# Optimization experiments

Hardware: AMD Instinct MI355X
Metric: run time of the kernel (lower is better)

Reference implementation:

```python
import jax, jax.numpy as jnp
import numpy as np

C1, C2, RATIO = 512, 256, 16

def setup_inputs() -> dict:
    key = jax.random.key(0)
    k1, k2, k3 = jax.random.split(key, 3)
    x = jax.random.normal(k1, (32, C1, 64, 64), dtype=jnp.float32)
    # torch Linear(c1, c1//ratio, bias=False): weight [c1//ratio, c1]
    w1 = jax.random.normal(k2, (C1 // RATIO, C1), dtype=jnp.float32) * (1.0 / np.sqrt(C1))
    w2 = jax.random.normal(k3, (C1, C1 // RATIO), dtype=jnp.float32) * (1.0 / np.sqrt(C1 // RATIO))
    return {"x": x, "w1": w1, "w2": w2}

def reference(x, w1, w2):
    b, c, h, w = x.shape
    # global average pool -> [b, c]
    y = jnp.mean(x, axis=(2, 3))
    # SE MLP: relu(y @ w1.T) @ w2.T, then sigmoid
    y = jax.nn.sigmoid(jnp.einsum('br,cr->bc', jax.nn.relu(jnp.einsum('bc,rc->br', y, w1)), w2))
    # descending sort indices over channels, keep top c2
    idx = jnp.argsort(-y, axis=1)[:, :C2]            # [b, c2] int
    # per-batch channel gather: out[b] = x[b, idx[b]]
    out = jnp.take_along_axis(x, idx[:, :, None, None], axis=1)  # [b, c2, h, w]
    return out
```

## Files before the change

kernel.cpp:

```cpp
#include <hip/hip_runtime.h>
#include <hip/hip_bf16.h>
#include <math.h>


#define C1 512
#define C2 256
#define CMID 32
#define HW 4096
#define B 32
#define W1PAD 516

typedef float f32x4 __attribute__((ext_vector_type(4)));

__device__ float g_y[B * C1];
__device__ int   g_idx[B * C2];

__global__ __launch_bounds__(256) void pool_np_kernel(const float* __restrict__ x) {
    int bc = blockIdx.x * 4 + (threadIdx.x >> 6);
    int L = threadIdx.x & 63;
    const float* a = x + (size_t)bc * HW;
    const float* base = a + (L >> 1) * 128 + (L & 1) * 4;
    f32x4 r = *(const f32x4*)base;
#pragma unroll
    for (int i = 1; i < 16; ++i) {
        f32x4 v = *(const f32x4*)(base + 8 * i);
        r.x = __fadd_rn(r.x, v.x);
        r.y = __fadd_rn(r.y, v.y);
        r.z = __fadd_rn(r.z, v.z);
        r.w = __fadd_rn(r.w, v.w);
    }
    float s = __fadd_rn(__fadd_rn(r.x, r.y), __fadd_rn(r.z, r.w));
    s = __fadd_rn(s, __shfl_xor(s, 1));
    s = __fadd_rn(s, __shfl_xor(s, 2));
    s = __fadd_rn(s, __shfl_xor(s, 4));
    s = __fadd_rn(s, __shfl_xor(s, 8));
    s = __fadd_rn(s, __shfl_xor(s, 16));
    s = __fadd_rn(s, __shfl_xor(s, 32));
    if (L == 0) g_y[bc] = __fdiv_rn(s, 4096.0f);
}

__global__ __launch_bounds__(512) void se_np_kernel(const float* __restrict__ w1,
                                                    const float* __restrict__ w2) {
    int b = blockIdx.x;
    int t = threadIdx.x;
    __shared__ float ys[C1];
    __shared__ float hs[CMID];
    __shared__ float ss[C1];
    __shared__ float w1s[CMID * W1PAD];

    f32x4 w2r[8];
#pragma unroll
    for (int i = 0; i < 8; ++i)
        w2r[i] = ((const f32x4*)(w2 + t * CMID))[i];

#pragma unroll
    for (int i = 0; i < 8; ++i) {
        int u = i * 512 + t;
        int row  = u >> 7;
        int col4 = u & 127;
        f32x4 v = ((const f32x4*)w1)[u];
        *(f32x4*)&w1s[row * W1PAD + col4 * 4] = v;
    }
    ys[t] = g_y[b * C1 + t];
    __syncthreads();

    if (t < CMID * 4) {
        int row = t >> 2, k = t & 3;
        const float* wr = &w1s[row * W1PAD];
        float Lk = 0.f;
#pragma unroll
        for (int c = 0; c < C1; c += 8) {
            Lk = __fadd_rn(Lk, __fmul_rn(ys[c + k],     wr[c + k]));
            Lk = __fadd_rn(Lk, __fmul_rn(ys[c + 4 + k], wr[c + 4 + k]));
        }
        Lk = __fadd_rn(Lk, __shfl_xor(Lk, 1));
        Lk = __fadd_rn(Lk, __shfl_xor(Lk, 2));
        if (k == 0) hs[row] = Lk > 0.0f ? Lk : 0.0f;
    }
    __syncthreads();

    {
        float L0 = 0.f, L1 = 0.f, L2 = 0.f, L3 = 0.f;
#pragma unroll
        for (int i = 0; i < 8; i += 2) {
            L0 = __fadd_rn(L0, __fmul_rn(hs[i * 4 + 0], w2r[i].x));
            L1 = __fadd_rn(L1, __fmul_rn(hs[i * 4 + 1], w2r[i].y));
            L2 = __fadd_rn(L2, __fmul_rn(hs[i * 4 + 2], w2r[i].z));
            L3 = __fadd_rn(L3, __fmul_rn(hs[i * 4 + 3], w2r[i].w));
            L0 = __fadd_rn(L0, __fmul_rn(hs[i * 4 + 4], w2r[i + 1].x));
            L1 = __fadd_rn(L1, __fmul_rn(hs[i * 4 + 5], w2r[i + 1].y));
            L2 = __fadd_rn(L2, __fmul_rn(hs[i * 4 + 6], w2r[i + 1].z));
            L3 = __fadd_rn(L3, __fmul_rn(hs[i * 4 + 7], w2r[i + 1].w));
        }
        float z = __fadd_rn(__fadd_rn(L0, L1), __fadd_rn(L2, L3));
        float e = (float)exp((double)(-z));
        ss[t] = __fdiv_rn(1.0f, __fadd_rn(1.0f, e));
    }
    __syncthreads();

    float sc = ss[t];
    int rank = 0;
#pragma unroll 8
    for (int c = 0; c < C1; ++c) {
        float v = ss[c];
        rank += (int)((v > sc) || (v == sc && c < t));
    }
    if (rank < C2) g_idx[b * C2 + rank] = t;
}

__global__ __launch_bounds__(256) void gather_kernel(const float* __restrict__ x,
                                                     float* __restrict__ out) {
    int bid  = blockIdx.x >> 1;
    int half = blockIdx.x & 1;
    int b = bid >> 8;
    int c = g_idx[bid];
    const f32x4* src = (const f32x4*)(x + ((size_t)(b * C1 + c)) * HW);
    f32x4* dst = (f32x4*)(out + (size_t)bid * HW);
    int j = half * 512 + threadIdx.x;
    f32x4 v0 = src[j];
    f32x4 v1 = src[j + 256];
    __builtin_nontemporal_store(v0, &dst[j]);
    __builtin_nontemporal_store(v1, &dst[j + 256]);
}

extern "C" void kernel_launch(void* const* d_in, const int* in_sizes, int n_in,
                              void* d_out, int out_size, void* d_ws, size_t ws_size,
                              hipStream_t stream) {
    const float* x  = (const float*)d_in[0];
    const float* w1 = (const float*)d_in[1];
    const float* w2 = (const float*)d_in[2];
    float* out = (float*)d_out;

    pool_np_kernel<<<B * C1 / 4, 256, 0, stream>>>(x);
    se_np_kernel<<<B, C1, 0, stream>>>(w1, w2);
    gather_kernel<<<B * C2 * 2, 256, 0, stream>>>(x, out);
}
```

Baseline: 100.7 us.

## Fuse SE MLP and top-k ranking into the gather kernel

Merges the SE/ranking kernel with the gather kernel so each gather block recomputes the channel scores and ranks locally in shared memory, dropping the global index buffer and one launch. The w1 shared-memory staging is removed and w1 is read directly from global memory. The cost is that the MLP, sigmoid and 512x512 rank comparison are repeated redundantly by every one of the 128 blocks per batch, adding substantial compute and cached weight traffic.

```diff
diff --git a/kernel.cpp b/kernel.cpp
--- a/kernel.cpp
+++ b/kernel.cpp
@@ -8,12 +8,10 @@
 #define CMID 32
 #define HW 4096
 #define B 32
-#define W1PAD 516
 
 typedef float f32x4 __attribute__((ext_vector_type(4)));
 
 __device__ float g_y[B * C1];
-__device__ int   g_idx[B * C2];
 
 __global__ __launch_bounds__(256) void pool_np_kernel(const float* __restrict__ x) {
     int bc = blockIdx.x * 4 + (threadIdx.x >> 6);
@@ -39,39 +37,33 @@
     if (L == 0) g_y[bc] = __fdiv_rn(s, 4096.0f);
 }
 
-__global__ __launch_bounds__(512) void se_np_kernel(const float* __restrict__ w1,
-                                                    const float* __restrict__ w2) {
-    int b = blockIdx.x;
+__global__ __launch_bounds__(512) void se_gather_kernel(const float* __restrict__ x,
+                                                        const float* __restrict__ w1,
+                                                        const float* __restrict__ w2,
+                                                        float* __restrict__ out) {
     int t = threadIdx.x;
+    int b = blockIdx.x >> 7;
     __shared__ float ys[C1];
     __shared__ float hs[CMID];
     __shared__ float ss[C1];
-    __shared__ float w1s[CMID * W1PAD];
+    __shared__ int   idx_l[C2];
 
     f32x4 w2r[8];
 #pragma unroll
     for (int i = 0; i < 8; ++i)
         w2r[i] = ((const f32x4*)(w2 + t * CMID))[i];
 
-#pragma unroll
-    for (int i = 0; i < 8; ++i) {
-        int u = i * 512 + t;
-        int row  = u >> 7;
-        int col4 = u & 127;
-        f32x4 v = ((const f32x4*)w1)[u];
-        *(f32x4*)&w1s[row * W1PAD + col4 * 4] = v;
-    }
     ys[t] = g_y[b * C1 + t];
     __syncthreads();
 
     if (t < CMID * 4) {
         int row = t >> 2, k = t & 3;
-        const float* wr = &w1s[row * W1PAD];
+        const float* v = w1 + row * C1;
         float Lk = 0.f;
 #pragma unroll
         for (int c = 0; c < C1; c += 8) {
-            Lk = __fadd_rn(Lk, __fmul_rn(ys[c + k],     wr[c + k]));
-            Lk = __fadd_rn(Lk, __fmul_rn(ys[c + 4 + k], wr[c + 4 + k]));
+            Lk = __fadd_rn(Lk, __fmul_rn(ys[c + k],     v[c + k]));
+            Lk = __fadd_rn(Lk, __fmul_rn(ys[c + 4 + k], v[c + 4 + k]));
         }
         Lk = __fadd_rn(Lk, __shfl_xor(Lk, 1));
         Lk = __fadd_rn(Lk, __shfl_xor(Lk, 2));
@@ -98,29 +90,29 @@
     }
     __syncthreads();
 
-    float sc = ss[t];
-    int rank = 0;
+    {
+        float sc = ss[t];
+        int rank = 0;
 #pragma unroll 8
-    for (int c = 0; c < C1; ++c) {
-        float v = ss[c];
-        rank += (int)((v > sc) || (v == sc && c < t));
+        for (int c = 0; c < C1; ++c) {
+            float v = ss[c];
+            rank += (int)((v > sc) || (v == sc && c < t));
+        }
+        if (rank < C2) idx_l[rank] = t;
     }
-    if (rank < C2) g_idx[b * C2 + rank] = t;
-}
+    __syncthreads();
 
-__global__ __launch_bounds__(256) void gather_kernel(const float* __restrict__ x,
-                                                     float* __restrict__ out) {
-    int bid  = blockIdx.x >> 1;
-    int half = blockIdx.x & 1;
-    int b = bid >> 8;
-    int c = g_idx[bid];
-    const f32x4* src = (const f32x4*)(x + ((size_t)(b * C1 + c)) * HW);
-    f32x4* dst = (f32x4*)(out + (size_t)bid * HW);
-    int j = half * 512 + threadIdx.x;
-    f32x4 v0 = src[j];
-    f32x4 v1 = src[j + 256];
-    __builtin_nontemporal_store(v0, &dst[j]);
-    __builtin_nontemporal_store(v1, &dst[j + 256]);
+#pragma unroll
+    for (int q = 0; q < 2; ++q) {
+        int bid = blockIdx.x * 2 + q;
+        int c = idx_l[bid & 255];
+        const f32x4* src = (const f32x4*)(x + ((size_t)(b * C1 + c)) * HW);
+        f32x4* dst = (f32x4*)(out + (size_t)bid * HW);
+        f32x4 v0 = src[t];
+        f32x4 v1 = src[t + 512];
+        __builtin_nontemporal_store(v0, &dst[t]);
+        __builtin_nontemporal_store(v1, &dst[t + 512]);
+    }
 }
 
 extern "C" void kernel_launch(void* const* d_in, const int* in_sizes, int n_in,
@@ -132,6 +124,5 @@
     float* out = (float*)d_out;
 
     pool_np_kernel<<<B * C1 / 4, 256, 0, stream>>>(x);
-    se_np_kernel<<<B, C1, 0, stream>>>(w1, w2);
-    gather_kernel<<<B * C2 * 2, 256, 0, stream>>>(x, out);
+    se_gather_kernel<<<B * C2 / 2, 512, 0, stream>>>(x, w1, w2, out);
 }
```

After: 218.4 us. +116.9%, slower.

## Split SE rank computation across 8 blocks per batch with atomic rank accumulation

Applied to the files above, without the earlier changes.

The SE/rank kernel now launches 8 blocks per batch. Each block recomputes the MLP and counts ranks over a 64-channel slice, then atomically adds its partial rank into a global per-channel rank array, which the pool kernel zeroes first. The gather kernel finds its source channel by scanning the rank array in shared memory and now copies a whole channel per 512-thread block. The aim is to cut the latency of the serial 512-iteration rank loop that ran on only 32 blocks. The cost is the MLP work repeated in every block, plus the atomics and a rank lookup in each gather block.

```diff
diff --git a/kernel.cpp b/kernel.cpp
--- a/kernel.cpp
+++ b/kernel.cpp
@@ -13,9 +13,11 @@
 typedef float f32x4 __attribute__((ext_vector_type(4)));
 
 __device__ float g_y[B * C1];
-__device__ int   g_idx[B * C2];
+__device__ int   g_rank[B * C1];
 
 __global__ __launch_bounds__(256) void pool_np_kernel(const float* __restrict__ x) {
+    if (blockIdx.x < 64) g_rank[blockIdx.x * 256 + threadIdx.x] = 0;
+
     int bc = blockIdx.x * 4 + (threadIdx.x >> 6);
     int L = threadIdx.x & 63;
     const float* a = x + (size_t)bc * HW;
@@ -39,9 +41,10 @@
     if (L == 0) g_y[bc] = __fdiv_rn(s, 4096.0f);
 }
 
-__global__ __launch_bounds__(512) void se_np_kernel(const float* __restrict__ w1,
-                                                    const float* __restrict__ w2) {
-    int b = blockIdx.x;
+__global__ __launch_bounds__(512) void se_rank_kernel(const float* __restrict__ w1,
+                                                      const float* __restrict__ w2) {
+    int b = blockIdx.x >> 3;
+    int j = blockIdx.x & 7;
     int t = threadIdx.x;
     __shared__ float ys[C1];
     __shared__ float hs[CMID];
@@ -98,29 +101,36 @@
     }
     __syncthreads();
 
-    float sc = ss[t];
-    int rank = 0;
-#pragma unroll 8
-    for (int c = 0; c < C1; ++c) {
-        float v = ss[c];
-        rank += (int)((v > sc) || (v == sc && c < t));
+    {
+        float sc = ss[t];
+        int c0 = j * 64;
+        int rank = 0;
+#pragma unroll 16
+        for (int c = c0; c < c0 + 64; ++c) {
+            float v = ss[c];
+            rank += (int)((v > sc) || (v == sc && c < t));
+        }
+        atomicAdd(&g_rank[b * C1 + t], rank);
     }
-    if (rank < C2) g_idx[b * C2 + rank] = t;
 }
 
-__global__ __launch_bounds__(256) void gather_kernel(const float* __restrict__ x,
+__global__ __launch_bounds__(512) void gather_kernel(const float* __restrict__ x,
                                                      float* __restrict__ out) {
-    int bid  = blockIdx.x >> 1;
-    int half = blockIdx.x & 1;
+    int bid = blockIdx.x;
     int b = bid >> 8;
-    int c = g_idx[bid];
+    int r = bid & 255;
+    int t = threadIdx.x;
+    __shared__ int win;
+    int rk = g_rank[b * C1 + t];
+    if (rk == r) win = t;
+    __syncthreads();
+    int c = win;
     const f32x4* src = (const f32x4*)(x + ((size_t)(b * C1 + c)) * HW);
     f32x4* dst = (f32x4*)(out + (size_t)bid * HW);
-    int j = half * 512 + threadIdx.x;
-    f32x4 v0 = src[j];
-    f32x4 v1 = src[j + 256];
-    __builtin_nontemporal_store(v0, &dst[j]);
-    __builtin_nontemporal_store(v1, &dst[j + 256]);
+    f32x4 v0 = src[t];
+    f32x4 v1 = src[t + 512];
+    __builtin_nontemporal_store(v0, &dst[t]);
+    __builtin_nontemporal_store(v1, &dst[t + 512]);
 }
 
 extern "C" void kernel_launch(void* const* d_in, const int* in_sizes, int n_in,
@@ -132,6 +142,6 @@
     float* out = (float*)d_out;
 
     pool_np_kernel<<<B * C1 / 4, 256, 0, stream>>>(x);
-    se_np_kernel<<<B, C1, 0, stream>>>(w1, w2);
-    gather_kernel<<<B * C2 * 2, 256, 0, stream>>>(x, out);
+    se_rank_kernel<<<B * 8, 512, 0, stream>>>(w1, w2);
+    gather_kernel<<<B * C2, 512, 0, stream>>>(x, out);
 }
```

Result: faster. 90.46 us, median of 2 (-10.2%).
